# Kernel tuning notes

Measured on AMD Instinct MI355X. Metric: run time of the kernel, lower is better.

Reference implementation:

```python
import jax, jax.numpy as jnp
import numpy as np

B, S, D = 32, 4096, 64          # batch, max seq len, input_dim
P, STRIDE, H = 8, 4, 512        # patch_size, patch_stride, hidden_size
T = (S - P) // STRIDE + 1       # static max token count (sample 0 has length S)
EPS = 1e-6


def setup_inputs() -> dict:
    key = jax.random.key(0)
    k1, k2, k3 = jax.random.split(key, 3)
    x = jax.random.normal(k1, (B, S, D), dtype=jnp.float32)
    lengths = jax.random.randint(k2, (B,), P, S + 1)
    lengths = lengths.at[0].set(S)  # at least one full-length sample -> max_tokens == T
    W = jax.random.normal(k3, (P * D, H), dtype=jnp.float32) / np.sqrt(P * D)
    b = jnp.zeros((H,), dtype=jnp.float32)
    scale = jnp.ones((H,), dtype=jnp.float32)  # RMSNorm scale
    return {"x": x, "lengths": lengths, "W": W, "b": b, "scale": scale}


def _patch(x, lengths):
    # number of tokens per sample: len(range(0, max(L-P+1, 1), STRIDE))
    n_tok = jnp.where(lengths >= P, (lengths - P) // STRIDE + 1, 1)  # [B]
    # gather positions for every (token, within-patch) slot
    pos = jnp.arange(T)[:, None] * STRIDE + jnp.arange(P)[None, :]   # [T, P]
    tokens = x[:, pos, :]                                            # [B, T, P, D]
    valid = (pos[None, :, :] < lengths[:, None, None]) \
          & (jnp.arange(T)[None, :, None] < n_tok[:, None, None])    # [B, T, P]
    tokens = jnp.where(valid[..., None], tokens, 0.0)
    return tokens.reshape(B, T, P * D), n_tok


def reference(x, lengths, W, b, scale):
    tokens, token_lengths = _patch(x, lengths)        # [B, T, P*D], [B]
    h = tokens @ W + b                                # proj -> [B, T, H]
    rms = jnp.sqrt(jnp.mean(h * h, axis=-1, keepdims=True) + EPS)
    hidden = h / rms * scale                          # RMSNorm
    return hidden, token_lengths, tokens
```

## Files before the change

### kernel.cpp

```cpp
#include <hip/hip_runtime.h>
#include <hip/hip_bf16.h>

constexpr int Bc = 32, Sc = 4096, Dc = 64, Pc = 8, STRIDEc = 4, Hc = 512;
constexpr int Tc = (Sc - Pc) / STRIDEc + 1;
constexpr int Kc = Pc * Dc;
constexpr float EPSc = 1e-6f;
constexpr int PITCH = 40;

typedef __bf16 bf16x8 __attribute__((ext_vector_type(8)));
typedef unsigned short ushort8 __attribute__((ext_vector_type(8)));
typedef float f32x4 __attribute__((ext_vector_type(4)));

__device__ __forceinline__ int n_tok_of(int len) {
    return (len >= Pc) ? ((len - Pc) / STRIDEc + 1) : 1;
}

__device__ __forceinline__ unsigned short f2bf(float f) {
    unsigned u = __builtin_bit_cast(unsigned, f);
    u = (u + 0x7FFFu + ((u >> 16) & 1u)) >> 16;
    return (unsigned short)u;
}

__global__ __launch_bounds__(256) void prep_kernel(
        const float* __restrict__ W, const int* __restrict__ lengths,
        unsigned short* __restrict__ Wt, float* __restrict__ out_tl) {
    __shared__ float tile[32][33];
    const int k0 = blockIdx.x * 32, n0 = blockIdx.y * 32;
    const int r = threadIdx.x >> 3, c = (threadIdx.x & 7) * 4;
    const float4 v = *(const float4*)(W + (size_t)(k0 + r) * Hc + n0 + c);
    tile[c + 0][r] = v.x;
    tile[c + 1][r] = v.y;
    tile[c + 2][r] = v.z;
    tile[c + 3][r] = v.w;
    __syncthreads();
    ushort4 o;
    o.x = f2bf(tile[r][c + 0]);
    o.y = f2bf(tile[r][c + 1]);
    o.z = f2bf(tile[r][c + 2]);
    o.w = f2bf(tile[r][c + 3]);
    *(ushort4*)(Wt + (size_t)blockIdx.x * (Hc * 32) + (size_t)(n0 + r) * 32 + c) = o;
    if (blockIdx.x == 0 && blockIdx.y == 0 && threadIdx.x < Bc)
        out_tl[threadIdx.x] = (float)n_tok_of(lengths[threadIdx.x]);
}

__global__ __launch_bounds__(256, 2) void fused_kernel(
        const float* __restrict__ x, const int* __restrict__ lengths,
        const unsigned short* __restrict__ Wt, const float* __restrict__ bias,
        const float* __restrict__ scale, float* __restrict__ hidden,
        float* __restrict__ tokens) {
    const int b  = blockIdx.y;
    const int t0 = ((b & 16) ? (15 - (int)blockIdx.x) : (int)blockIdx.x) * 64;
    const int len = lengths[b];
    const int ntok = n_tok_of(len);
    const int tid = threadIdx.x;

    float* tokb = tokens + (size_t)b * Tc * Kc;

    if (t0 >= ntok) {
        __shared__ float red[4];
        const int w = tid >> 6, lane = tid & 63;
        const float2 b2 = *(const float2*)(bias + tid * 2);
        float s = b2.x * b2.x + b2.y * b2.y;
#pragma unroll
        for (int off = 32; off; off >>= 1) s += __shfl_xor(s, off);
        if (lane == 0) red[w] = s;
        __syncthreads();
        const float rstd0 = rsqrtf((red[0] + red[1] + red[2] + red[3])
                                   * (1.0f / (float)Hc) + EPSc);
        const int c4 = (tid & 127) * 4;
        const f32x4 cvec = *(const f32x4*)(bias + c4) * rstd0
                         * *(const f32x4*)(scale + c4);
        const f32x4 z = {0.f, 0.f, 0.f, 0.f};
        float* hidb = hidden + ((size_t)b * Tc + t0) * Hc;
        float* tokp = tokb + (size_t)t0 * Kc;
        const int r0 = tid >> 7;
#pragma unroll 8
        for (int rr = r0; rr < 64; rr += 2) {
            if (t0 + rr < Tc) {
                __builtin_nontemporal_store(cvec, (f32x4*)(hidb + (size_t)rr * Hc + c4));
                __builtin_nontemporal_store(z,    (f32x4*)(tokp + (size_t)rr * Kc + c4));
            }
        }
        return;
    }

    __shared__ unsigned short As[64 * PITCH];
    __shared__ unsigned short Bs[512 * PITCH];
    __shared__ float ssbuf[4][64];

    const int w    = tid >> 6;
    const int lane = tid & 63;
    const int l15  = lane & 15;
    const int quad = lane >> 4;

    f32x4 acc[4][8];
#pragma unroll
    for (int tt = 0; tt < 4; ++tt)
#pragma unroll
        for (int ct = 0; ct < 8; ++ct) acc[tt][ct] = (f32x4){0.f, 0.f, 0.f, 0.f};

    const float* xb = x + (size_t)b * (Sc * Dc);

    int   a_r[2], a_c[2];  bool a_tv[2], a_lv[2];  const float* a_src[2];
#pragma unroll
    for (int it = 0; it < 2; ++it) {
        const int l = tid + it * 256;
        a_r[it] = l >> 3;
        a_c[it] = (l & 7) * 4;
        const int t = t0 + a_r[it];
        a_tv[it] = (t < Tc);
        a_lv[it] = (t < ntok);
        a_src[it] = xb + (size_t)t * (STRIDEc * Dc);
    }

    float4  ra[2];
    ushort8 rb[8];

#pragma unroll
    for (int it = 0; it < 2; ++it) {
        ra[it] = make_float4(0.f, 0.f, 0.f, 0.f);
        if (a_lv[it]) ra[it] = *(const float4*)(a_src[it] + a_c[it]);
    }
#pragma unroll
    for (int it = 0; it < 8; ++it)
        rb[it] = *(const ushort8*)(Wt + (size_t)(tid + it * 256) * 8);

    for (int step = 0; step < 16; ++step) {
        const int k0 = step * 32;
        if (step) __syncthreads();

#pragma unroll
        for (int it = 0; it < 2; ++it) {
            const float4 v = ra[it];
            if (a_tv[it])
                *(float4*)(tokb + (size_t)(t0 + a_r[it]) * Kc + k0 + a_c[it]) = v;
            ushort4 h4;
            h4.x = f2bf(v.x); h4.y = f2bf(v.y); h4.z = f2bf(v.z); h4.w = f2bf(v.w);
            *(ushort4*)(As + a_r[it] * PITCH + a_c[it]) = h4;
        }
#pragma unroll
        for (int it = 0; it < 8; ++it) {
            const int cc = tid + it * 256;
            *(ushort8*)(Bs + (cc >> 2) * PITCH + (cc & 3) * 8) = rb[it];
        }
        __syncthreads();

        if (step < 15) {
            const int kn = k0 + 32;
#pragma unroll
            for (int it = 0; it < 2; ++it) {
                ra[it] = make_float4(0.f, 0.f, 0.f, 0.f);
                if (a_lv[it]) ra[it] = *(const float4*)(a_src[it] + kn + a_c[it]);
            }
            const unsigned short* wsrc = Wt + (size_t)(step + 1) * (Hc * 32);
#pragma unroll
            for (int it = 0; it < 8; ++it)
                rb[it] = *(const ushort8*)(wsrc + (size_t)(tid + it * 256) * 8);
        }

        bf16x8 btok[4];
#pragma unroll
        for (int tt = 0; tt < 4; ++tt)
            btok[tt] = __builtin_bit_cast(bf16x8,
                *(const ushort8*)(As + (tt * 16 + l15) * PITCH + quad * 8));
#pragma unroll
        for (int ct = 0; ct < 8; ++ct) {
            bf16x8 aW = __builtin_bit_cast(bf16x8,
                *(const ushort8*)(Bs + (w * 128 + ct * 16 + l15) * PITCH + quad * 8));
#pragma unroll
            for (int tt = 0; tt < 4; ++tt)
                acc[tt][ct] = __builtin_amdgcn_mfma_f32_16x16x32_bf16(
                    aW, btok[tt], acc[tt][ct], 0, 0, 0);
        }
    }

    float ss[4] = {0.f, 0.f, 0.f, 0.f};
#pragma unroll
    for (int ct = 0; ct < 8; ++ct) {
        const f32x4 b4 = *(const f32x4*)(bias + w * 128 + ct * 16 + quad * 4);
#pragma unroll
        for (int tt = 0; tt < 4; ++tt) {
            f32x4 h = acc[tt][ct] + b4;
            acc[tt][ct] = h;
            ss[tt] += h[0] * h[0] + h[1] * h[1] + h[2] * h[2] + h[3] * h[3];
        }
    }
#pragma unroll
    for (int tt = 0; tt < 4; ++tt) {
        float s = ss[tt];
        s += __shfl_xor(s, 16);
        s += __shfl_xor(s, 32);
        if (quad == 0) ssbuf[w][tt * 16 + l15] = s;
    }
    __syncthreads();
    float rstd[4];
#pragma unroll
    for (int tt = 0; tt < 4; ++tt) {
        const int r = tt * 16 + l15;
        const float tot = ssbuf[0][r] + ssbuf[1][r] + ssbuf[2][r] + ssbuf[3][r];
        rstd[tt] = rsqrtf(tot * (1.0f / (float)Hc) + EPSc);
    }
#pragma unroll
    for (int ct = 0; ct < 8; ++ct) {
        const f32x4 s4 = *(const f32x4*)(scale + w * 128 + ct * 16 + quad * 4);
#pragma unroll
        for (int tt = 0; tt < 4; ++tt) {
            const int t = t0 + tt * 16 + l15;
            if (t < Tc) {
                f32x4 o = acc[tt][ct] * rstd[tt] * s4;
                *(f32x4*)(hidden + ((size_t)b * Tc + t) * Hc
                          + w * 128 + ct * 16 + quad * 4) = o;
            }
        }
    }
}

extern "C" void kernel_launch(void* const* d_in, const int* in_sizes, int n_in,
                              void* d_out, int out_size, void* d_ws, size_t ws_size,
                              hipStream_t stream) {
    const float* x       = (const float*)d_in[0];
    const int*   lengths = (const int*)d_in[1];
    const float* W       = (const float*)d_in[2];
    const float* bias    = (const float*)d_in[3];
    const float* scale   = (const float*)d_in[4];

    const size_t BTH = (size_t)Bc * Tc * Hc;
    float* out    = (float*)d_out;
    float* hidden = out;
    float* tl     = out + BTH;
    float* tokens = out + BTH + Bc;

    unsigned short* Wt = (unsigned short*)d_ws;

    {
        dim3 grid(Hc / 32, Hc / 32);
        prep_kernel<<<grid, 256, 0, stream>>>(W, lengths, Wt, tl);
    }
    {
        dim3 grid(16, Bc);
        fused_kernel<<<grid, 256, 0, stream>>>(x, lengths, Wt, bias, scale,
                                               hidden, tokens);
    }
}
```

Measured before the change: 187.1 us.

## Schedule fused tiles by valid-token count to balance GPU workload

The prep kernel now counting-sorts all 512 (batch, token-tile) work items by how many valid tokens each holds. It writes a schedule that places the heaviest tiles first, with the order for the second half of the slots reversed. The fused kernel reads its (b, t0) from this schedule instead of a fixed mapping. The aim is to even out per-CU load between full GEMM tiles and cheap fill-only tiles, at the cost of extra work in one prep block and an indirect lookup at kernel start.

```diff
diff --git a/kernel.cpp b/kernel.cpp
--- a/kernel.cpp
+++ b/kernel.cpp
@@ -6,6 +6,7 @@
 constexpr int Kc = Pc * Dc;
 constexpr float EPSc = 1e-6f;
 constexpr int PITCH = 40;
+constexpr size_t WT_BYTES = 512 * 512 * 2;
 
 typedef __bf16 bf16x8 __attribute__((ext_vector_type(8)));
 typedef unsigned short ushort8 __attribute__((ext_vector_type(8)));
@@ -23,7 +24,8 @@
 
 __global__ __launch_bounds__(256) void prep_kernel(
         const float* __restrict__ W, const int* __restrict__ lengths,
-        unsigned short* __restrict__ Wt, float* __restrict__ out_tl) {
+        unsigned short* __restrict__ Wt, int* __restrict__ sched,
+        float* __restrict__ out_tl) {
     __shared__ float tile[32][33];
     const int k0 = blockIdx.x * 32, n0 = blockIdx.y * 32;
     const int r = threadIdx.x >> 3, c = (threadIdx.x & 7) * 4;
@@ -39,20 +41,58 @@
     o.z = f2bf(tile[r][c + 2]);
     o.w = f2bf(tile[r][c + 3]);
     *(ushort4*)(Wt + (size_t)blockIdx.x * (Hc * 32) + (size_t)(n0 + r) * 32 + c) = o;
-    if (blockIdx.x == 0 && blockIdx.y == 0 && threadIdx.x < Bc)
-        out_tl[threadIdx.x] = (float)n_tok_of(lengths[threadIdx.x]);
+
+    if (blockIdx.x == 0 && blockIdx.y == 0) {
+        const int tid = threadIdx.x;
+        __shared__ int sntok[32];
+        __shared__ int scnt[65];
+        __shared__ int soff[65];
+        __shared__ int ssorted[512];
+        if (tid < Bc) {
+            const int nt = n_tok_of(lengths[tid]);
+            sntok[tid] = nt;
+            out_tl[tid] = (float)nt;
+        }
+        if (tid < 65) scnt[tid] = 0;
+        __syncthreads();
+#pragma unroll
+        for (int i = tid; i < 512; i += 256) {
+            int cst = sntok[i & 31] - (i >> 5) * 64;
+            cst = cst < 0 ? 0 : (cst > 64 ? 64 : cst);
+            atomicAdd(&scnt[64 - cst], 1);
+        }
+        __syncthreads();
+        if (tid == 0) {
+            int acc = 0;
+            for (int k = 0; k < 65; ++k) { soff[k] = acc; acc += scnt[k]; }
+        }
+        __syncthreads();
+#pragma unroll
+        for (int i = tid; i < 512; i += 256) {
+            int cst = sntok[i & 31] - (i >> 5) * 64;
+            cst = cst < 0 ? 0 : (cst > 64 ? 64 : cst);
+            const int pos = atomicAdd(&soff[64 - cst], 1);
+            ssorted[pos] = i;
+        }
+        __syncthreads();
+#pragma unroll
+        for (int s = tid; s < 512; s += 256)
+            sched[s] = (s < 256) ? ssorted[s] : ssorted[767 - s];
+    }
 }
 
 __global__ __launch_bounds__(256, 2) void fused_kernel(
         const float* __restrict__ x, const int* __restrict__ lengths,
         const unsigned short* __restrict__ Wt, const float* __restrict__ bias,
-        const float* __restrict__ scale, float* __restrict__ hidden,
-        float* __restrict__ tokens) {
-    const int b  = blockIdx.y;
-    const int t0 = ((b & 16) ? (15 - (int)blockIdx.x) : (int)blockIdx.x) * 64;
-    const int len = lengths[b];
+        const float* __restrict__ scale, const int* __restrict__ sched,
+        float* __restrict__ hidden, float* __restrict__ tokens) {
+    const int slot = (int)blockIdx.y * 16 + (int)blockIdx.x;
+    const int idx  = sched[slot];
+    const int b    = idx & 31;
+    const int t0   = (idx >> 5) * 64;
+    const int len  = lengths[b];
     const int ntok = n_tok_of(len);
-    const int tid = threadIdx.x;
+    const int tid  = threadIdx.x;
 
     float* tokb = tokens + (size_t)b * Tc * Kc;
 
@@ -231,14 +271,15 @@
     float* tokens = out + BTH + Bc;
 
     unsigned short* Wt = (unsigned short*)d_ws;
+    int* sched = (int*)((char*)d_ws + WT_BYTES);
 
     {
         dim3 grid(Hc / 32, Hc / 32);
-        prep_kernel<<<grid, 256, 0, stream>>>(W, lengths, Wt, tl);
+        prep_kernel<<<grid, 256, 0, stream>>>(W, lengths, Wt, sched, tl);
     }
     {
         dim3 grid(16, Bc);
         fused_kernel<<<grid, 256, 0, stream>>>(x, lengths, Wt, bias, scale,
-                                               hidden, tokens);
-    }
-}
+                                               sched, hidden, tokens);
+    }
+}
```

Result: no change. 188.7 us (+0.8%).

## Split tokens output writes into separate blocks from GEMM blocks

Applied to the files above, without the earlier changes.

The grid becomes 1024 one-dimensional blocks. The first 512 do the projection and RMSNorm GEMM, and the other 512 write the tokens tensor, copying straight from x, along with the constant hidden rows for padded tokens. GEMM blocks no longer store tokens inside their k-loop, and blocks past the sample length now exit early. This separates the memory-bound copy from the MFMA work so the two can overlap across CUs, at the cost of reading x twice and launching more blocks.

```diff
diff --git a/kernel.cpp b/kernel.cpp
--- a/kernel.cpp
+++ b/kernel.cpp
@@ -48,15 +48,15 @@
         const unsigned short* __restrict__ Wt, const float* __restrict__ bias,
         const float* __restrict__ scale, float* __restrict__ hidden,
         float* __restrict__ tokens) {
-    const int b  = blockIdx.y;
-    const int t0 = ((b & 16) ? (15 - (int)blockIdx.x) : (int)blockIdx.x) * 64;
-    const int len = lengths[b];
-    const int ntok = n_tok_of(len);
+    const int id  = (int)blockIdx.x;
     const int tid = threadIdx.x;
 
-    float* tokb = tokens + (size_t)b * Tc * Kc;
-
-    if (t0 >= ntok) {
+    if (id >= 512) {
+        const int sid = id - 512;
+        const int b   = sid & 31;
+        const int t0  = (sid >> 5) * 64;
+        const int ntok = n_tok_of(lengths[b]);
+
         __shared__ float red[4];
         const int w = tid >> 6, lane = tid & 63;
         const float2 b2 = *(const float2*)(bias + tid * 2);
@@ -67,22 +67,42 @@
         __syncthreads();
         const float rstd0 = rsqrtf((red[0] + red[1] + red[2] + red[3])
                                    * (1.0f / (float)Hc) + EPSc);
-        const int c4 = (tid & 127) * 4;
-        const f32x4 cvec = *(const f32x4*)(bias + c4) * rstd0
-                         * *(const f32x4*)(scale + c4);
-        const f32x4 z = {0.f, 0.f, 0.f, 0.f};
-        float* hidb = hidden + ((size_t)b * Tc + t0) * Hc;
-        float* tokp = tokb + (size_t)t0 * Kc;
-        const int r0 = tid >> 7;
-#pragma unroll 8
-        for (int rr = r0; rr < 64; rr += 2) {
-            if (t0 + rr < Tc) {
-                __builtin_nontemporal_store(cvec, (f32x4*)(hidb + (size_t)rr * Hc + c4));
-                __builtin_nontemporal_store(z,    (f32x4*)(tokp + (size_t)rr * Kc + c4));
+
+        const int r = tid >> 2;
+        const int q = tid & 3;
+        const int t = t0 + r;
+        if (t < Tc) {
+            float* tokp = tokens + ((size_t)b * Tc + t) * Kc + q * 128;
+            if (t < ntok) {
+                const float* xs = x + (size_t)b * (Sc * Dc) + (size_t)t * (STRIDEc * Dc)
+                                + q * 128;
+#pragma unroll
+                for (int j = 0; j < 32; ++j) {
+                    const f32x4 v = *(const f32x4*)(xs + j * 4);
+                    __builtin_nontemporal_store(v, (f32x4*)(tokp + j * 4));
+                }
+            } else {
+                const f32x4 z = {0.f, 0.f, 0.f, 0.f};
+#pragma unroll
+                for (int j = 0; j < 32; ++j)
+                    __builtin_nontemporal_store(z, (f32x4*)(tokp + j * 4));
+                float* hidp = hidden + ((size_t)b * Tc + t) * Hc + q * 128;
+#pragma unroll
+                for (int j = 0; j < 32; ++j) {
+                    const int c = q * 128 + j * 4;
+                    const f32x4 cv = *(const f32x4*)(bias + c) * rstd0
+                                   * *(const f32x4*)(scale + c);
+                    __builtin_nontemporal_store(cv, (f32x4*)(hidp + j * 4));
+                }
             }
         }
         return;
     }
+
+    const int b  = id & 31;
+    const int t0 = (id >> 5) * 64;
+    const int ntok = n_tok_of(lengths[b]);
+    if (t0 >= ntok) return;
 
     __shared__ unsigned short As[64 * PITCH];
     __shared__ unsigned short Bs[512 * PITCH];
@@ -101,14 +121,13 @@
 
     const float* xb = x + (size_t)b * (Sc * Dc);
 
-    int   a_r[2], a_c[2];  bool a_tv[2], a_lv[2];  const float* a_src[2];
+    int   a_r[2], a_c[2];  bool a_lv[2];  const float* a_src[2];
 #pragma unroll
     for (int it = 0; it < 2; ++it) {
         const int l = tid + it * 256;
         a_r[it] = l >> 3;
         a_c[it] = (l & 7) * 4;
         const int t = t0 + a_r[it];
-        a_tv[it] = (t < Tc);
         a_lv[it] = (t < ntok);
         a_src[it] = xb + (size_t)t * (STRIDEc * Dc);
     }
@@ -126,14 +145,11 @@
         rb[it] = *(const ushort8*)(Wt + (size_t)(tid + it * 256) * 8);
 
     for (int step = 0; step < 16; ++step) {
-        const int k0 = step * 32;
         if (step) __syncthreads();
 
 #pragma unroll
         for (int it = 0; it < 2; ++it) {
             const float4 v = ra[it];
-            if (a_tv[it])
-                *(float4*)(tokb + (size_t)(t0 + a_r[it]) * Kc + k0 + a_c[it]) = v;
             ushort4 h4;
             h4.x = f2bf(v.x); h4.y = f2bf(v.y); h4.z = f2bf(v.z); h4.w = f2bf(v.w);
             *(ushort4*)(As + a_r[it] * PITCH + a_c[it]) = h4;
@@ -146,7 +162,7 @@
         __syncthreads();
 
         if (step < 15) {
-            const int kn = k0 + 32;
+            const int kn = step * 32 + 32;
 #pragma unroll
             for (int it = 0; it < 2; ++it) {
                 ra[it] = make_float4(0.f, 0.f, 0.f, 0.f);
@@ -206,7 +222,7 @@
 #pragma unroll
         for (int tt = 0; tt < 4; ++tt) {
             const int t = t0 + tt * 16 + l15;
-            if (t < Tc) {
+            if (t < ntok) {
                 f32x4 o = acc[tt][ct] * rstd[tt] * s4;
                 *(f32x4*)(hidden + ((size_t)b * Tc + t) * Hc
                           + w * 128 + ct * 16 + quad * 4) = o;
@@ -237,8 +253,7 @@
         prep_kernel<<<grid, 256, 0, stream>>>(W, lengths, Wt, tl);
     }
     {
-        dim3 grid(16, Bc);
-        fused_kernel<<<grid, 256, 0, stream>>>(x, lengths, Wt, bias, scale,
-                                               hidden, tokens);
-    }
-}
+        fused_kernel<<<dim3(1024), 256, 0, stream>>>(x, lengths, Wt, bias, scale,
+                                                     hidden, tokens);
+    }
+}
```

Result: slower. 400.6 us (+114.1%).
